# Performance work log

Hardware: AMD Instinct MI355X
Metric: run time of the kernel (lower is better)

Reference implementation:

```python
import jax, jax.numpy as jnp
import numpy as np

B = 4096                      # flattened tokens
IN_MODES = (16, 16, 16)       # auto_shape(4096, d=3)
OUT_MODES = (16, 16, 16)
RANK = 8                      # tt ranks: (1, 8, 8, 1)


def setup_inputs() -> dict:
    key = jax.random.key(0)
    ks = jax.random.split(key, 4)
    ranks = (1, RANK, RANK, 1)
    x = jax.random.normal(ks[0], (B, int(np.prod(IN_MODES))), dtype=jnp.float32)
    cores = []
    for i in range(3):
        shp = (ranks[i], IN_MODES[i], OUT_MODES[i], ranks[i + 1])
        # glorot-style variance for TT cores (t3.glorot_initializer analogue)
        std = float(np.sqrt(2.0 / (ranks[i] * IN_MODES[i] + OUT_MODES[i] * ranks[i + 1])))
        cores.append(jax.random.normal(ks[i + 1], shp, dtype=jnp.float32) * std)
    bias = 0.001 * jnp.ones((int(np.prod(OUT_MODES)),), dtype=jnp.float32)
    return {"x": x, "core0": cores[0], "core1": cores[1], "core2": cores[2], "bias": bias}


def _tt_matmul(x, core0, core1, core2):
    # dense_tt_matmul: y = x @ W, W the TT-matrix with cores (r_{k-1}, m_k, n_k, r_k)
    Bn = x.shape[0]
    data = x.reshape((Bn,) + IN_MODES)                     # [B, m1, m2, m3]
    # core0 has leading rank 1 -> squeeze it
    res = jnp.einsum('bmxy,mnr->bxynr', data, core0[0])    # [B, m2, m3, n1, r1]
    res = jnp.einsum('bmynr,rmfs->bynfs', res, core1)      # [B, m3, n1, n2, r2]
    res = jnp.einsum('bmnpe,emf->bnpf', res, core2[..., 0])  # [B, n1, n2, n3]
    return res.reshape(Bn, -1)                             # [B, n1*n2*n3]


def reference(x, core0, core1, core2, bias):
    return _tt_matmul(x, core0, core1, core2) + bias
```

## Files before the change

kernel.cpp:

```cpp
#include <hip/hip_runtime.h>


typedef __attribute__((ext_vector_type(8))) short bf16x8;
typedef __attribute__((ext_vector_type(4))) float f32x4;

__device__ __forceinline__ unsigned short f2bf(float f) {
    unsigned u = __builtin_bit_cast(unsigned, f);
    u += 0x7FFFu + ((u >> 16) & 1u);
    return (unsigned short)(u >> 16);
}

__device__ __forceinline__ unsigned f2bf_pk(float lo, float hi) {
#if __has_builtin(__builtin_amdgcn_cvt_pk_bf16_f32)
    typedef __attribute__((ext_vector_type(2))) __bf16 bf2;
    bf2 r = __builtin_amdgcn_cvt_pk_bf16_f32(lo, hi);
    return __builtin_bit_cast(unsigned, r);
#else
    return (unsigned)f2bf(lo) | ((unsigned)f2bf(hi) << 16);
#endif
}

union BF8 { bf16x8 v; unsigned short s[8]; unsigned u[4]; };
union U2  { uint2 d; unsigned u[2]; };

#define S2 136
#define S3 2208
#define R1 40
#define R2 672

#define MFMA32 __builtin_amdgcn_mfma_f32_16x16x32_bf16

__global__ __launch_bounds__(512, 4) void tt_mfma3_v5(
    const float* __restrict__ x, const float* __restrict__ c0,
    const float* __restrict__ c1, const float* __restrict__ c2,
    const float* __restrict__ bias, float* __restrict__ out)
{
    __shared__ __align__(16) unsigned short sT1[4 * S3];
    __shared__ __align__(16) unsigned short sT2[16 * R2];

    const int tid  = threadIdx.x;
    const int w    = tid >> 6;
    const int lane = tid & 63;
    const int q    = lane >> 4;
    const int c    = lane & 15;
    const int qh   = q >> 1, ql = q & 1;

    const int ct1  = w & 3;
    const int rtg1 = w >> 2;
    const int rp2  = w & 3;
    const int vp2  = w >> 2;

    unsigned short* const w1p = &sT1[(c >> 2) * S3 + (ct1 * 4 + (c & 3)) * S2
                                     + (rtg1 * 8 + qh) * 8 + 4 * ql];
    const unsigned short* const r2p = &sT1[(vp2 * 2) * S3 + q * S2 + c * 8];
    unsigned short* const w2p = &sT2[(rp2 * 4 + qh) * R2 + c * R1
                                     + vp2 * 16 + 4 * ql];
    const unsigned short* const r3p = &sT2[(w * 2) * R2 + c * R1 + q * 8];
    const int xcol = ct1 * 64 + (c & 3) * 16 + (c >> 2) * 4;

    const f32x4 zero = {0.f, 0.f, 0.f, 0.f};

    BF8 xpk[4];
    #pragma unroll
    for (int s = 0; s < 4; ++s)
        xpk[s].u[0] = xpk[s].u[1] = xpk[s].u[2] = xpk[s].u[3] = 0;

    auto issue_x = [&](int tb) {
        if (q < 2) {
            const float* xb = x + (size_t)(blockIdx.x * 8 + tb) * 4096;
            f32x4 t[8];
            #pragma unroll
            for (int j = 0; j < 8; ++j)
                t[j] = *(const f32x4*)&xb[(q * 8 + j) * 256 + xcol];
            #pragma unroll
            for (int s = 0; s < 4; ++s) {
                #pragma unroll
                for (int u = 0; u < 4; ++u)
                    xpk[s].u[u] = f2bf_pk(t[2 * u][s], t[2 * u + 1][s]);
            }
        }
    };

    issue_x(0);

    BF8 a0[4];
    #pragma unroll
    for (int i = 0; i < 4; ++i) {
        if (q < 2) {
            const int n1 = (rtg1 * 4 + i) * 2 + (c >> 3), r1 = c & 7;
            const float* p = &c0[(q * 8) * 128 + n1 * 8 + r1];
            #pragma unroll
            for (int u = 0; u < 4; ++u)
                a0[i].u[u] = f2bf_pk(p[(2 * u) * 128], p[(2 * u + 1) * 128]);
        } else {
            a0[i].u[0] = a0[i].u[1] = a0[i].u[2] = a0[i].u[3] = 0;
        }
    }
    BF8 aF[2][4];
    #pragma unroll
    for (int i = 0; i < 2; ++i) {
        const int n2 = (rp2 * 2 + i) * 2 + (c >> 3), r2 = c & 7;
        #pragma unroll
        for (int k4 = 0; k4 < 4; ++k4) {
            const float* p = &c1[(k4 * 4 + q) * 128 + n2 * 8 + r2];
            #pragma unroll
            for (int u = 0; u < 4; ++u)
                aF[i][k4].u[u] = f2bf_pk(p[(2 * u) * 2048], p[(2 * u + 1) * 2048]);
        }
    }
    BF8 a2[4];
    #pragma unroll
    for (int s = 0; s < 4; ++s) {
        const float* p = &c2[(q * 4 + s) * 16 + c];
        #pragma unroll
        for (int u = 0; u < 4; ++u)
            a2[s].u[u] = f2bf_pk(p[(2 * u) * 256], p[(2 * u + 1) * 256]);
    }

    auto G1 = [&](int s2) {
        #pragma unroll
        for (int i = 0; i < 4; ++i) {
            f32x4 d = MFMA32(a0[i].v, xpk[s2].v, zero, 0, 0, 0);
            U2 t; t.u[0] = f2bf_pk(d[0], d[1]); t.u[1] = f2bf_pk(d[2], d[3]);
            *(uint2*)(w1p + i * 16) = t.d;
        }
    };

    for (int tok = 0; tok < 8; ++tok) {
        const int b = blockIdx.x * 8 + tok;

        f32x4 acc3[2] = {zero, zero};

        G1(0);
        #pragma unroll
        for (int s = 0; s < 4; ++s) {
            __syncthreads();
            if (s == 3 && tok < 7) issue_x(tok + 1);
            f32x4 acc2[2][2] = {{zero, zero}, {zero, zero}};
            __builtin_amdgcn_s_setprio(1);
            #pragma unroll
            for (int k4 = 0; k4 < 4; ++k4) {
                bf16x8 b0 = *(const bf16x8*)(r2p + k4 * 544);
                bf16x8 b1 = *(const bf16x8*)(r2p + S3 + k4 * 544);
                #pragma unroll
                for (int i = 0; i < 2; ++i) {
                    acc2[i][0] = MFMA32(aF[i][k4].v, b0, acc2[i][0], 0, 0, 0);
                    acc2[i][1] = MFMA32(aF[i][k4].v, b1, acc2[i][1], 0, 0, 0);
                }
            }
            __builtin_amdgcn_s_setprio(0);
            #pragma unroll
            for (int i = 0; i < 2; ++i) {
                #pragma unroll
                for (int j = 0; j < 2; ++j) {
                    U2 t;
                    t.u[0] = f2bf_pk(acc2[i][j][0], acc2[i][j][1]);
                    t.u[1] = f2bf_pk(acc2[i][j][2], acc2[i][j][3]);
                    *(uint2*)(w2p + i * 1344 + j * 8) = t.d;
                }
            }
            __syncthreads();
            {
                bf16x8 b0 = *(const bf16x8*)(r3p);
                bf16x8 b1 = *(const bf16x8*)(r3p + R2);
                acc3[0] = MFMA32(a2[s].v, b0, acc3[0], 0, 0, 0);
                acc3[1] = MFMA32(a2[s].v, b1, acc3[1], 0, 0, 0);
            }
            if (s < 3) G1(s + 1);
        }

        float* outb = out + (size_t)b * 4096;
        #pragma unroll
        for (int t = 0; t < 2; ++t) {
            const int idx = c * 256 + (w * 2 + t) * 16 + 4 * q;
            f32x4 bv = *(const f32x4*)&bias[idx];
            f32x4 o = acc3[t] + bv;
            *(f32x4*)&outb[idx] = o;
        }
    }
}

extern "C" void kernel_launch(void* const* d_in, const int* in_sizes, int n_in,
                              void* d_out, int out_size, void* d_ws, size_t ws_size,
                              hipStream_t stream) {
    const float* x    = (const float*)d_in[0];
    const float* c0   = (const float*)d_in[1];
    const float* c1   = (const float*)d_in[2];
    const float* c2   = (const float*)d_in[3];
    const float* bias = (const float*)d_in[4];
    float* out = (float*)d_out;

    tt_mfma3_v5<<<512, 512, 0, stream>>>(x, c0, c1, c2, bias, out);
}
```

Before: 171.3 us.

## Double-buffer LDS stages to software-pipeline TT contractions with one barrier per step

```diff
diff --git a/kernel.cpp b/kernel.cpp
--- a/kernel.cpp
+++ b/kernel.cpp
@@ -30,13 +30,13 @@
 
 #define MFMA32 __builtin_amdgcn_mfma_f32_16x16x32_bf16
 
-__global__ __launch_bounds__(512, 4) void tt_mfma3_v5(
+__global__ __launch_bounds__(512, 4) void tt_mfma3_v6(
     const float* __restrict__ x, const float* __restrict__ c0,
     const float* __restrict__ c1, const float* __restrict__ c2,
     const float* __restrict__ bias, float* __restrict__ out)
 {
-    __shared__ __align__(16) unsigned short sT1[4 * S3];
-    __shared__ __align__(16) unsigned short sT2[16 * R2];
+    __shared__ __align__(16) unsigned short sT1[2][4 * S3];
+    __shared__ __align__(16) unsigned short sT2[2][16 * R2];
 
     const int tid  = threadIdx.x;
     const int w    = tid >> 6;
@@ -50,13 +50,11 @@
     const int rp2  = w & 3;
     const int vp2  = w >> 2;
 
-    unsigned short* const w1p = &sT1[(c >> 2) * S3 + (ct1 * 4 + (c & 3)) * S2
-                                     + (rtg1 * 8 + qh) * 8 + 4 * ql];
-    const unsigned short* const r2p = &sT1[(vp2 * 2) * S3 + q * S2 + c * 8];
-    unsigned short* const w2p = &sT2[(rp2 * 4 + qh) * R2 + c * R1
-                                     + vp2 * 16 + 4 * ql];
-    const unsigned short* const r3p = &sT2[(w * 2) * R2 + c * R1 + q * 8];
-    const int xcol = ct1 * 64 + (c & 3) * 16 + (c >> 2) * 4;
+    const int w1off = (c >> 2) * S3 + (ct1 * 4 + (c & 3)) * S2 + (rtg1 * 8 + qh) * 8 + 4 * ql;
+    const int r2off = (vp2 * 2) * S3 + q * S2 + c * 8;
+    const int w2off = (rp2 * 4 + qh) * R2 + c * R1 + vp2 * 16 + 4 * ql;
+    const int r3off = (w * 2) * R2 + c * R1 + q * 8;
+    const int xcol  = ct1 * 64 + (c & 3) * 16 + (c >> 2) * 4;
 
     const f32x4 zero = {0.f, 0.f, 0.f, 0.f};
 
@@ -117,59 +115,52 @@
             a2[s].u[u] = f2bf_pk(p[(2 * u) * 256], p[(2 * u + 1) * 256]);
     }
 
-    auto G1 = [&](int s2) {
+    f32x4 acc3[2] = {zero, zero};
+
+    auto G1 = [&](int buf, int s2) {
         #pragma unroll
         for (int i = 0; i < 4; ++i) {
             f32x4 d = MFMA32(a0[i].v, xpk[s2].v, zero, 0, 0, 0);
             U2 t; t.u[0] = f2bf_pk(d[0], d[1]); t.u[1] = f2bf_pk(d[2], d[3]);
-            *(uint2*)(w1p + i * 16) = t.d;
-        }
-    };
-
-    for (int tok = 0; tok < 8; ++tok) {
-        const int b = blockIdx.x * 8 + tok;
-
-        f32x4 acc3[2] = {zero, zero};
-
-        G1(0);
-        #pragma unroll
-        for (int s = 0; s < 4; ++s) {
-            __syncthreads();
-            if (s == 3 && tok < 7) issue_x(tok + 1);
-            f32x4 acc2[2][2] = {{zero, zero}, {zero, zero}};
-            __builtin_amdgcn_s_setprio(1);
-            #pragma unroll
-            for (int k4 = 0; k4 < 4; ++k4) {
-                bf16x8 b0 = *(const bf16x8*)(r2p + k4 * 544);
-                bf16x8 b1 = *(const bf16x8*)(r2p + S3 + k4 * 544);
-                #pragma unroll
-                for (int i = 0; i < 2; ++i) {
-                    acc2[i][0] = MFMA32(aF[i][k4].v, b0, acc2[i][0], 0, 0, 0);
-                    acc2[i][1] = MFMA32(aF[i][k4].v, b1, acc2[i][1], 0, 0, 0);
-                }
-            }
-            __builtin_amdgcn_s_setprio(0);
+            *(uint2*)&sT1[buf][w1off + i * 16] = t.d;
+        }
+    };
+
+    auto G2 = [&](int buf) {
+        f32x4 acc2[2][2] = {{zero, zero}, {zero, zero}};
+        __builtin_amdgcn_s_setprio(1);
+        #pragma unroll
+        for (int k4 = 0; k4 < 4; ++k4) {
+            bf16x8 b0 = *(const bf16x8*)&sT1[buf][r2off + k4 * 544];
+            bf16x8 b1 = *(const bf16x8*)&sT1[buf][r2off + S3 + k4 * 544];
             #pragma unroll
             for (int i = 0; i < 2; ++i) {
-                #pragma unroll
-                for (int j = 0; j < 2; ++j) {
-                    U2 t;
-                    t.u[0] = f2bf_pk(acc2[i][j][0], acc2[i][j][1]);
-                    t.u[1] = f2bf_pk(acc2[i][j][2], acc2[i][j][3]);
-                    *(uint2*)(w2p + i * 1344 + j * 8) = t.d;
-                }
-            }
-            __syncthreads();
-            {
-                bf16x8 b0 = *(const bf16x8*)(r3p);
-                bf16x8 b1 = *(const bf16x8*)(r3p + R2);
-                acc3[0] = MFMA32(a2[s].v, b0, acc3[0], 0, 0, 0);
-                acc3[1] = MFMA32(a2[s].v, b1, acc3[1], 0, 0, 0);
-            }
-            if (s < 3) G1(s + 1);
-        }
-
-        float* outb = out + (size_t)b * 4096;
+                acc2[i][0] = MFMA32(aF[i][k4].v, b0, acc2[i][0], 0, 0, 0);
+                acc2[i][1] = MFMA32(aF[i][k4].v, b1, acc2[i][1], 0, 0, 0);
+            }
+        }
+        __builtin_amdgcn_s_setprio(0);
+        #pragma unroll
+        for (int i = 0; i < 2; ++i) {
+            #pragma unroll
+            for (int j = 0; j < 2; ++j) {
+                U2 t;
+                t.u[0] = f2bf_pk(acc2[i][j][0], acc2[i][j][1]);
+                t.u[1] = f2bf_pk(acc2[i][j][2], acc2[i][j][3]);
+                *(uint2*)&sT2[buf][w2off + i * 1344 + j * 8] = t.d;
+            }
+        }
+    };
+
+    auto G3 = [&](int buf, int sp) {
+        bf16x8 b0 = *(const bf16x8*)&sT2[buf][r3off];
+        bf16x8 b1 = *(const bf16x8*)&sT2[buf][r3off + R2];
+        acc3[0] = MFMA32(a2[sp].v, b0, acc3[0], 0, 0, 0);
+        acc3[1] = MFMA32(a2[sp].v, b1, acc3[1], 0, 0, 0);
+    };
+
+    auto epilogue = [&](int tb) {
+        float* outb = out + (size_t)(blockIdx.x * 8 + tb) * 4096;
         #pragma unroll
         for (int t = 0; t < 2; ++t) {
             const int idx = c * 256 + (w * 2 + t) * 16 + 4 * q;
@@ -177,7 +168,33 @@
             f32x4 o = acc3[t] + bv;
             *(f32x4*)&outb[idx] = o;
         }
-    }
+    };
+
+    G1(0, 0);
+    __syncthreads();
+
+    for (int tok = 0; tok < 8; ++tok) {
+        #pragma unroll
+        for (int s = 0; s < 4; ++s) {
+            const int pb = s & 1;
+            if (s == 0) {
+                if (tok > 0) {
+                    G3(1, 3);
+                    epilogue(tok - 1);
+                    acc3[0] = zero; acc3[1] = zero;
+                }
+            } else {
+                G3(pb ^ 1, s - 1);
+            }
+            if (s == 3 && tok < 7) issue_x(tok + 1);
+            G2(pb);
+            if (s < 3)           G1(pb ^ 1, s + 1);
+            else if (tok < 7)    G1(pb ^ 1, 0);
+            __syncthreads();
+        }
+    }
+    G3(1, 3);
+    epilogue(7);
 }
 
 extern "C" void kernel_launch(void* const* d_in, const int* in_sizes, int n_in,
@@ -190,5 +207,5 @@
     const float* bias = (const float*)d_in[4];
     float* out = (float*)d_out;
 
-    tt_mfma3_v5<<<512, 512, 0, stream>>>(x, c0, c1, c2, bias, out);
-}
+    tt_mfma3_v6<<<512, 512, 0, stream>>>(x, c0, c1, c2, bias, out);
+}
```

Measured after the change: 181.1 us. 5.7% more time.

## Process two m3 slices per barrier phase with doubled LDS staging

Applied to the files above, without the earlier changes.

```diff
diff --git a/kernel.cpp b/kernel.cpp
--- a/kernel.cpp
+++ b/kernel.cpp
@@ -25,17 +25,17 @@
 
 #define S2 136
 #define S3 2208
-#define R1 40
-#define R2 672
+#define R1 72
+#define R2 1184
 
 #define MFMA32 __builtin_amdgcn_mfma_f32_16x16x32_bf16
 
-__global__ __launch_bounds__(512, 4) void tt_mfma3_v5(
+__global__ __launch_bounds__(512, 4) void tt_mfma3_v8(
     const float* __restrict__ x, const float* __restrict__ c0,
     const float* __restrict__ c1, const float* __restrict__ c2,
     const float* __restrict__ bias, float* __restrict__ out)
 {
-    __shared__ __align__(16) unsigned short sT1[4 * S3];
+    __shared__ __align__(16) unsigned short sT1[8 * S3];
     __shared__ __align__(16) unsigned short sT2[16 * R2];
 
     const int tid  = threadIdx.x;
@@ -50,33 +50,33 @@
     const int rp2  = w & 3;
     const int vp2  = w >> 2;
 
-    unsigned short* const w1p = &sT1[(c >> 2) * S3 + (ct1 * 4 + (c & 3)) * S2
-                                     + (rtg1 * 8 + qh) * 8 + 4 * ql];
-    const unsigned short* const r2p = &sT1[(vp2 * 2) * S3 + q * S2 + c * 8];
-    unsigned short* const w2p = &sT2[(rp2 * 4 + qh) * R2 + c * R1
-                                     + vp2 * 16 + 4 * ql];
-    const unsigned short* const r3p = &sT2[(w * 2) * R2 + c * R1 + q * 8];
-    const int xcol = ct1 * 64 + (c & 3) * 16 + (c >> 2) * 4;
+    const int w1off = (c >> 2) * S3 + (ct1 * 4 + (c & 3)) * S2 + (rtg1 * 8 + qh) * 8 + 4 * ql;
+    const int r2off = (vp2 * 2) * S3 + q * S2 + c * 8;
+    const int w2off = (rp2 * 4 + qh) * R2 + c * R1 + vp2 * 16 + 4 * ql;
+    const int r3off = (w * 2) * R2 + c * R1 + q * 8;
+    const int xcol  = ct1 * 64 + (c & 3) * 16 + (c >> 2) * 4;
 
     const f32x4 zero = {0.f, 0.f, 0.f, 0.f};
 
-    BF8 xpk[4];
-    #pragma unroll
-    for (int s = 0; s < 4; ++s)
-        xpk[s].u[0] = xpk[s].u[1] = xpk[s].u[2] = xpk[s].u[3] = 0;
+    BF8 xpk[2][2];
+    #pragma unroll
+    for (int S = 0; S < 2; ++S)
+        #pragma unroll
+        for (int h = 0; h < 2; ++h)
+            xpk[S][h].u[0] = xpk[S][h].u[1] = xpk[S][h].u[2] = xpk[S][h].u[3] = 0;
 
     auto issue_x = [&](int tb) {
         if (q < 2) {
             const float* xb = x + (size_t)(blockIdx.x * 8 + tb) * 4096;
-            f32x4 t[8];
-            #pragma unroll
-            for (int j = 0; j < 8; ++j)
-                t[j] = *(const f32x4*)&xb[(q * 8 + j) * 256 + xcol];
-            #pragma unroll
-            for (int s = 0; s < 4; ++s) {
-                #pragma unroll
-                for (int u = 0; u < 4; ++u)
-                    xpk[s].u[u] = f2bf_pk(t[2 * u][s], t[2 * u + 1][s]);
+            #pragma unroll
+            for (int u = 0; u < 4; ++u) {
+                f32x4 t0 = *(const f32x4*)&xb[(q * 8 + 2 * u) * 256 + xcol];
+                f32x4 t1 = *(const f32x4*)&xb[(q * 8 + 2 * u + 1) * 256 + xcol];
+                #pragma unroll
+                for (int S = 0; S < 2; ++S)
+                    #pragma unroll
+                    for (int h = 0; h < 2; ++h)
+                        xpk[S][h].u[u] = f2bf_pk(t0[2 * h + S], t1[2 * h + S]);
             }
         }
     };
@@ -108,21 +108,27 @@
                 aF[i][k4].u[u] = f2bf_pk(p[(2 * u) * 2048], p[(2 * u + 1) * 2048]);
         }
     }
-    BF8 a2[4];
-    #pragma unroll
-    for (int s = 0; s < 4; ++s) {
-        const float* p = &c2[(q * 4 + s) * 16 + c];
-        #pragma unroll
-        for (int u = 0; u < 4; ++u)
-            a2[s].u[u] = f2bf_pk(p[(2 * u) * 256], p[(2 * u + 1) * 256]);
-    }
-
-    auto G1 = [&](int s2) {
-        #pragma unroll
-        for (int i = 0; i < 4; ++i) {
-            f32x4 d = MFMA32(a0[i].v, xpk[s2].v, zero, 0, 0, 0);
-            U2 t; t.u[0] = f2bf_pk(d[0], d[1]); t.u[1] = f2bf_pk(d[2], d[3]);
-            *(uint2*)(w1p + i * 16) = t.d;
+    BF8 a2[2][2];
+    #pragma unroll
+    for (int S = 0; S < 2; ++S) {
+        #pragma unroll
+        for (int h = 0; h < 2; ++h) {
+            const float* p = &c2[(q * 4 + 2 * h + S) * 16 + c];
+            #pragma unroll
+            for (int u = 0; u < 4; ++u)
+                a2[S][h].u[u] = f2bf_pk(p[(2 * u) * 256], p[(2 * u + 1) * 256]);
+        }
+    }
+
+    auto G1 = [&](int S) {
+        #pragma unroll
+        for (int h = 0; h < 2; ++h) {
+            #pragma unroll
+            for (int i = 0; i < 4; ++i) {
+                f32x4 d = MFMA32(a0[i].v, xpk[S][h].v, zero, 0, 0, 0);
+                U2 t; t.u[0] = f2bf_pk(d[0], d[1]); t.u[1] = f2bf_pk(d[2], d[3]);
+                *(uint2*)&sT1[w1off + h * 4 * S3 + i * 16] = t.d;
+            }
         }
     };
 
@@ -133,40 +139,45 @@
 
         G1(0);
         #pragma unroll
-        for (int s = 0; s < 4; ++s) {
+        for (int S = 0; S < 2; ++S) {
             __syncthreads();
-            if (s == 3 && tok < 7) issue_x(tok + 1);
-            f32x4 acc2[2][2] = {{zero, zero}, {zero, zero}};
-            __builtin_amdgcn_s_setprio(1);
-            #pragma unroll
-            for (int k4 = 0; k4 < 4; ++k4) {
-                bf16x8 b0 = *(const bf16x8*)(r2p + k4 * 544);
-                bf16x8 b1 = *(const bf16x8*)(r2p + S3 + k4 * 544);
+            if (S == 1 && tok < 7) issue_x(tok + 1);
+            #pragma unroll
+            for (int h = 0; h < 2; ++h) {
+                f32x4 acc2[2][2] = {{zero, zero}, {zero, zero}};
+                __builtin_amdgcn_s_setprio(1);
+                #pragma unroll
+                for (int k4 = 0; k4 < 4; ++k4) {
+                    bf16x8 b0 = *(const bf16x8*)&sT1[r2off + h * 4 * S3 + k4 * 544];
+                    bf16x8 b1 = *(const bf16x8*)&sT1[r2off + h * 4 * S3 + S3 + k4 * 544];
+                    #pragma unroll
+                    for (int i = 0; i < 2; ++i) {
+                        acc2[i][0] = MFMA32(aF[i][k4].v, b0, acc2[i][0], 0, 0, 0);
+                        acc2[i][1] = MFMA32(aF[i][k4].v, b1, acc2[i][1], 0, 0, 0);
+                    }
+                }
+                __builtin_amdgcn_s_setprio(0);
                 #pragma unroll
                 for (int i = 0; i < 2; ++i) {
-                    acc2[i][0] = MFMA32(aF[i][k4].v, b0, acc2[i][0], 0, 0, 0);
-                    acc2[i][1] = MFMA32(aF[i][k4].v, b1, acc2[i][1], 0, 0, 0);
+                    #pragma unroll
+                    for (int j = 0; j < 2; ++j) {
+                        U2 t;
+                        t.u[0] = f2bf_pk(acc2[i][j][0], acc2[i][j][1]);
+                        t.u[1] = f2bf_pk(acc2[i][j][2], acc2[i][j][3]);
+                        *(uint2*)&sT2[w2off + i * 2 * R2 + h * 32 + j * 8] = t.d;
+                    }
                 }
             }
-            __builtin_amdgcn_s_setprio(0);
-            #pragma unroll
-            for (int i = 0; i < 2; ++i) {
-                #pragma unroll
-                for (int j = 0; j < 2; ++j) {
-                    U2 t;
-                    t.u[0] = f2bf_pk(acc2[i][j][0], acc2[i][j][1]);
-                    t.u[1] = f2bf_pk(acc2[i][j][2], acc2[i][j][3]);
-                    *(uint2*)(w2p + i * 1344 + j * 8) = t.d;
+            __syncthreads();
+            #pragma unroll
+            for (int t = 0; t < 2; ++t) {
+                #pragma unroll
+                for (int h = 0; h < 2; ++h) {
+                    bf16x8 b0 = *(const bf16x8*)&sT2[r3off + t * R2 + h * 32];
+                    acc3[t] = MFMA32(a2[S][h].v, b0, acc3[t], 0, 0, 0);
                 }
             }
-            __syncthreads();
-            {
-                bf16x8 b0 = *(const bf16x8*)(r3p);
-                bf16x8 b1 = *(const bf16x8*)(r3p + R2);
-                acc3[0] = MFMA32(a2[s].v, b0, acc3[0], 0, 0, 0);
-                acc3[1] = MFMA32(a2[s].v, b1, acc3[1], 0, 0, 0);
-            }
-            if (s < 3) G1(s + 1);
+            if (S == 0) G1(1);
         }
 
         float* outb = out + (size_t)b * 4096;
@@ -190,5 +201,5 @@
     const float* bias = (const float*)d_in[4];
     float* out = (float*)d_out;
 
-    tt_mfma3_v5<<<512, 512, 0, stream>>>(x, c0, c1, c2, bias, out);
-}
+    tt_mfma3_v8<<<512, 512, 0, stream>>>(x, c0, c1, c2, bias, out);
+}
```

Measured after the change: 179.6 us. 1.05x slower.
